# Kernel optimization log

Hardware: AMD Instinct MI355X
Metric: run time of the kernel (lower is better)

The kernel has to match this reference:

```python
import jax, jax.numpy as jnp
import numpy as np

CAP_FACTOR = 1.25


def _moe_top1(x, wg, w1, b1, w2, b2):
    """Top-1 switch MoE with capacity-based token dropping.
    x: [T, d]; wg: [d, E]; w1: [E, d, f]; b1: [E, f]; w2: [E, f, d]; b2: [E, d].
    """
    T, d = x.shape
    E = wg.shape[1]
    cap = int(CAP_FACTOR * T / E)
    probs = jax.nn.softmax(x @ wg, axis=-1)            # [T, E]
    idx = jnp.argmax(probs, axis=-1)                   # [T] expert assignment
    gate = jnp.max(probs, axis=-1)                     # [T] gate prob
    oh = jax.nn.one_hot(idx, E, dtype=jnp.int32)       # [T, E]
    # position of each token within its expert's buffer
    pos = (jnp.cumsum(oh, axis=0) * oh).sum(-1) - 1    # [T]
    keep = pos < cap                                   # drop tokens over capacity
    pos_w = jnp.where(keep, pos, cap)                  # dropped -> overflow slot
    # dispatch: scatter tokens into per-expert buffers [E, cap+1, d]
    buf = jnp.zeros((E, cap + 1, d), dtype=x.dtype).at[idx, pos_w].set(x)
    buf = buf[:, :cap]                                 # slice off overflow slot
    # grouped expert FFN
    h = jax.nn.relu(jnp.einsum('ecd,edf->ecf', buf, w1) + b1[:, None, :])
    eo = jnp.einsum('ecf,efd->ecd', h, w2) + b2[:, None, :]
    # combine: gather each token's expert output, scale by gate prob, zero dropped
    pos_g = jnp.minimum(pos_w, cap - 1)
    out = eo[idx, pos_g] * (gate * keep.astype(x.dtype))[:, None]
    return out


def setup_inputs():
    key = jax.random.key(0)
    ks = jax.random.split(key, 12)
    B, S, d, dff, E1, E2 = 8, 2048, 1024, 4096, 8, 16
    s = lambda fan: np.float32(1.0 / np.sqrt(fan))
    return dict(
        x=jax.random.normal(ks[0], (B, S, d), jnp.float32),
        y=jax.random.randint(ks[1], (B,), 0, d),
        wg1=jax.random.normal(ks[2], (d, E1), jnp.float32) * s(d),
        w1a=jax.random.normal(ks[3], (E1, d, dff), jnp.float32) * s(d),
        b1a=jnp.zeros((E1, dff), jnp.float32),
        w2a=jax.random.normal(ks[4], (E1, dff, d), jnp.float32) * s(dff),
        b2a=jnp.zeros((E1, d), jnp.float32),
        wg2=jax.random.normal(ks[5], (d, E2), jnp.float32) * s(d),
        w1b=jax.random.normal(ks[6], (E2, d, dff), jnp.float32) * s(d),
        b1b=jnp.zeros((E2, dff), jnp.float32),
        w2b=jax.random.normal(ks[7], (E2, dff, d), jnp.float32) * s(dff),
        b2b=jnp.zeros((E2, d), jnp.float32),
    )


def reference(x, y, wg1, w1a, b1a, w2a, b2a, wg2, w1b, b1b, w2b, b2b):
    B, S, d = x.shape
    xf = x.reshape(B * S, d)
    m1 = _moe_top1(xf, wg1, w1a, b1a, w2a, b2a)        # moe1(x)
    m2 = _moe_top1(m1, wg2, w1b, b1b, w2b, b2b)        # moe2(moe_out)
    resid = x + m2.reshape(B, S, d)                    # residual add
    sent = resid.mean(axis=1)                          # [B, d] mean-pool -> logits
    logp = jax.nn.log_softmax(sent, axis=-1)
    return -logp[jnp.arange(B), y].mean()              # cross-entropy loss
```

## Files before the change

### kernel.cpp

```cpp
#include <hip/hip_runtime.h>
#include <hip/hip_bf16.h>
#include <cstdint>
#include <cstddef>

#define B_    8
#define S_    2048
#define D_    1024
#define DFF_  4096
#define E1_   8
#define E2_   16
#define T_    (B_*S_)
#define CAP1_ 2560
#define CAP2_ 1280
#define EC_   20480

typedef float f32x4 __attribute__((ext_vector_type(4)));

__device__ __forceinline__ unsigned int pk4fp8(float a, float b, float c, float d) {
  int r = __builtin_amdgcn_cvt_pk_fp8_f32(a, b, 0, false);
  r = __builtin_amdgcn_cvt_pk_fp8_f32(c, d, r, true);
  return (unsigned int)r;
}

template<int E>
__global__ __launch_bounds__(256)
void gate_kernel(const float* __restrict__ X, const float* __restrict__ WG,
                 int* __restrict__ idxO, float* __restrict__ gateO) {
  const int lane = threadIdx.x & 63;
  const int wv   = threadIdx.x >> 6;
  const int t    = blockIdx.x * 4 + wv;
  const float* xr = X + (size_t)t * D_;
  float acc[E];
#pragma unroll
  for (int e = 0; e < E; ++e) acc[e] = 0.f;
#pragma unroll
  for (int i = 0; i < 4; ++i) {
    float4 xv = *(const float4*)(xr + i * 256 + lane * 4);
    int kb = i * 256 + lane * 4;
#pragma unroll
    for (int j = 0; j < 4; ++j) {
      float xs = (&xv.x)[j];
      const float* wr = WG + (size_t)(kb + j) * E;
#pragma unroll
      for (int e = 0; e < E; ++e) acc[e] += xs * wr[e];
    }
  }
#pragma unroll
  for (int e = 0; e < E; ++e) {
    float v = acc[e];
#pragma unroll
    for (int s = 32; s >= 1; s >>= 1) v += __shfl_xor(v, s, 64);
    acc[e] = v;
  }
  if (lane == 0) {
    float mx = acc[0]; int mi = 0;
#pragma unroll
    for (int e = 1; e < E; ++e) if (acc[e] > mx) { mx = acc[e]; mi = e; }
    float s = 0.f;
#pragma unroll
    for (int e = 0; e < E; ++e) s += expf(acc[e] - mx);
    idxO[t]  = mi;
    gateO[t] = 1.0f / s;
  }
}

__global__ __launch_bounds__(1024)
void scan_kernel(const int* __restrict__ idx, int E, int cap,
                 int* __restrict__ pos, int* __restrict__ kept) {
  __shared__ int cnt[16][17];
  __shared__ int gbase[16];
  const int tid = threadIdx.x;
  const int w = tid >> 6, lane = tid & 63;
  if (tid < E) gbase[tid] = 0;
  __syncthreads();
  const unsigned long long lt = (lane == 63) ? 0xFFFFFFFFFFFFFFFFull >> 1
                                             : ((1ull << lane) - 1ull);
  for (int it = 0; it < T_ / 1024; ++it) {
    int t = it * 1024 + tid;
    int mi = idx[t];
    int rank = 0;
    for (int e = 0; e < E; ++e) {
      unsigned long long m = __ballot(mi == e);
      if (lane == 0) cnt[w][e] = __popcll(m);
      if (mi == e) rank = __popcll(m & lt);
    }
    __syncthreads();
    int off = 0;
    for (int w2 = 0; w2 < w; ++w2) off += cnt[w2][mi];
    pos[t] = gbase[mi] + off + rank;
    __syncthreads();
    if (tid < E) {
      int tot = 0;
      for (int w2 = 0; w2 < 16; ++w2) tot += cnt[w2][tid];
      gbase[tid] += tot;
    }
    __syncthreads();
  }
  if (tid < E) kept[tid] = min(gbase[tid], cap);
}

__global__ __launch_bounds__(64)
void scatter_kernel(const float* __restrict__ X, const int* __restrict__ idx,
                    const int* __restrict__ pos, int cap,
                    unsigned char* __restrict__ xbuf, int* __restrict__ tokmap,
                    float* __restrict__ mzero) {
  const int t = blockIdx.x;
  const int lane = threadIdx.x;
  const int p = pos[t];
  if (p < cap) {
    const size_t dst = ((size_t)idx[t] * cap + p) * D_;
    const float* xr = X + (size_t)t * D_;
#pragma unroll
    for (int i = 0; i < 4; ++i) {
      float4 v = *(const float4*)(xr + i * 256 + lane * 4);
      *(unsigned int*)(xbuf + dst + i * 256 + lane * 4) = pk4fp8(v.x, v.y, v.z, v.w);
    }
    if (lane == 0) tokmap[(size_t)idx[t] * cap + p] = t;
  } else {
    float4 z = {0.f, 0.f, 0.f, 0.f};
    float* mr = mzero + (size_t)t * D_;
#pragma unroll
    for (int i = 0; i < 4; ++i) *(float4*)(mr + i * 256 + lane * 4) = z;
  }
}

__global__ __launch_bounds__(256)
void wtrans_kernel(const float* __restrict__ src, unsigned char* __restrict__ dst,
                   int K, int N) {
  __shared__ float t[64][65];
  const int tid = threadIdx.x;
  const size_t eo = (size_t)blockIdx.z * K * N;
  const int k0 = blockIdx.y * 64, n0 = blockIdx.x * 64;
  const float* s = src + eo + (size_t)k0 * N + n0;
  unsigned char* d = dst + eo + (size_t)n0 * K + k0;
#pragma unroll
  for (int i = 0; i < 4; ++i) {
    int k = i * 16 + (tid >> 4);
    int n4 = (tid & 15) * 4;
    float4 v = *(const float4*)(s + (size_t)k * N + n4);
    t[k][n4] = v.x; t[k][n4 + 1] = v.y; t[k][n4 + 2] = v.z; t[k][n4 + 3] = v.w;
  }
  __syncthreads();
#pragma unroll
  for (int i = 0; i < 4; ++i) {
    int n = i * 16 + (tid >> 4);
    int k4 = (tid & 15) * 4;
    *(unsigned int*)(d + (size_t)n * K + k4) =
        pk4fp8(t[k4][n], t[k4 + 1][n], t[k4 + 2][n], t[k4 + 3][n]);
  }
}

#define STG(BASEPTR, H, KT, SLOT) do {                                          \
    const unsigned char* _s = (BASEPTR) + (size_t)((H) * 128) * K + (KT) + st_off; \
    __builtin_amdgcn_global_load_lds((const __attribute__((address_space(1))) void*)_s, \
        (__attribute__((address_space(3))) void*)(smem + (SLOT) + dst0), 16, 0, 0);   \
    __builtin_amdgcn_global_load_lds((const __attribute__((address_space(1))) void*)(_s + (size_t)64 * K), \
        (__attribute__((address_space(3))) void*)(smem + (SLOT) + 8192 + dst0), 16, 0, 0); \
  } while (0)

#define RDA(BUF, MH) do { _Pragma("unroll")                                     \
    for (int m_ = 0; m_ < 4; ++m_) {                                            \
      const char* _p = smem + (BUF) * 65536 + aslot + ((MH) * 4 + m_) * 2048 + vaf; \
      _Pragma("unroll") for (int k_ = 0; k_ < 4; ++k_)                          \
        af[m_][k_] = *(const long long*)(_p + (((2 * k_ + c0) ^ swz7) << 4)); } } while (0)

#define RDB01(BUF, DEST) do { _Pragma("unroll")                                 \
    for (int j_ = 0; j_ < 2; ++j_) {                                            \
      const char* _p = smem + (BUF) * 65536 + bslot + j_ * 2048 + vbf;          \
      _Pragma("unroll") for (int k_ = 0; k_ < 4; ++k_)                          \
        DEST[j_][k_] = *(const long long*)(_p + (((2 * k_ + c0) ^ swz7) << 4)); } } while (0)

#define RDB23(BUF) do { _Pragma("unroll")                                       \
    for (int j_ = 0; j_ < 2; ++j_) {                                            \
      const char* _p = smem + (BUF) * 65536 + bslot + (2 + j_) * 2048 + vbf;    \
      _Pragma("unroll") for (int k_ = 0; k_ < 4; ++k_)                          \
        bfb[j_][k_] = *(const long long*)(_p + (((2 * k_ + c0) ^ swz7) << 4)); } } while (0)

#define QUADN0(MH, BA) do {                                                     \
    __builtin_amdgcn_s_setprio(1);                                              \
    _Pragma("unroll") for (int m_ = 0; m_ < 4; ++m_)                            \
    _Pragma("unroll") for (int j_ = 0; j_ < 2; ++j_)                            \
    _Pragma("unroll") for (int k_ = 0; k_ < 4; ++k_)                            \
      acc[(MH) * 4 + m_][j_] = __builtin_amdgcn_mfma_f32_16x16x32_fp8_fp8(      \
          af[m_][k_], BA[j_][k_], acc[(MH) * 4 + m_][j_], 0, 0, 0);             \
    __builtin_amdgcn_s_setprio(0);                                              \
  } while (0)

#define QUADN1(MH) do {                                                         \
    __builtin_amdgcn_s_setprio(1);                                              \
    _Pragma("unroll") for (int m_ = 0; m_ < 4; ++m_)                            \
    _Pragma("unroll") for (int j_ = 0; j_ < 2; ++j_)                            \
    _Pragma("unroll") for (int k_ = 0; k_ < 4; ++k_)                            \
      acc[(MH) * 4 + m_][2 + j_] = __builtin_amdgcn_mfma_f32_16x16x32_fp8_fp8(  \
          af[m_][k_], bfb[j_][k_], acc[(MH) * 4 + m_][2 + j_], 0, 0, 0);        \
    __builtin_amdgcn_s_setprio(0);                                              \
  } while (0)

#define SB0   __builtin_amdgcn_sched_barrier(0)
#define BAR   __builtin_amdgcn_s_barrier()
#define VM6   do { asm volatile("s_waitcnt vmcnt(6)" ::: "memory"); SB0; } while (0)
#define VM8   do { asm volatile("s_waitcnt vmcnt(8)" ::: "memory"); SB0; } while (0)
#define VM0   do { asm volatile("s_waitcnt vmcnt(0)" ::: "memory"); SB0; } while (0)

template<int MODE>
__global__ __launch_bounds__(512, 2)
void moe_gemm(const unsigned char* __restrict__ A,
              const unsigned char* __restrict__ BT,
              const float* __restrict__ bias, int K, int N, int cap, int nbcnt,
              int ntl,
              const int* __restrict__ kept,
              unsigned char* __restrict__ Hout, float* __restrict__ Mout,
              const int* __restrict__ tokmap, const float* __restrict__ gate,
              const float* __restrict__ tsrc, unsigned char* __restrict__ tdst,
              int tK, int tN, int tE, int nwrk) {
  __shared__ char smem[131072];
  const int tid  = threadIdx.x;

  if (tsrc != nullptr && (int)blockIdx.x < nwrk) {
    const int ntn = tN >> 7, ntk = tK >> 7;
    const int tiles = tE * ntk * ntn;
    const int krow = tid >> 2;
    const int kq   = (tid & 3) * 32;
    for (int t = blockIdx.x; t < tiles; t += nwrk) {
      const int e2 = t / (ntk * ntn), rm = t - e2 * (ntk * ntn);
      const int k0 = (rm / ntn) << 7, n0 = (rm - (rm / ntn) * ntn) << 7;
      const float* s = tsrc + (size_t)e2 * tK * tN + (size_t)(k0 + krow) * tN + n0 + kq;
#pragma unroll
      for (int j = 0; j < 8; ++j) {
        float4 v = *(const float4*)(s + j * 4);
        unsigned int q = pk4fp8(v.x, v.y, v.z, v.w);
#pragma unroll
        for (int b = 0; b < 4; ++b)
          smem[(kq + j * 4 + b) * 128 + krow] = (char)((q >> (8 * b)) & 0xff);
      }
      __syncthreads();
      unsigned char* d = tdst + (size_t)e2 * tK * tN + (size_t)(n0 + krow) * tK + k0 + kq;
      *(uint4*)(d)      = *(const uint4*)(smem + krow * 128 + kq);
      *(uint4*)(d + 16) = *(const uint4*)(smem + krow * 128 + kq + 16);
      __syncthreads();
    }
    return;
  }

  const int gbid = (int)blockIdx.x - (tsrc ? nwrk : 0);
  const int lane = tid & 63;
  const int wv   = tid >> 6;
  const int wr   = wv >> 2;
  const int wc   = wv & 3;

  const int wg  = (gbid & 7) * (ntl >> 3) + (gbid >> 3);
  const int per_grp = nbcnt * 4;
  const int grp = wg / per_grp;
  const int rem = wg - grp * per_grp;
  const int mb  = grp * 4 + (rem & 3);
  const int nb  = rem >> 2;

  const int e  = (mb * 256) / cap;
  const int r0 = mb * 256 - e * cap;
  const int kept_e = kept[e];
  if (r0 >= kept_e) return;
  const unsigned char* Ab = A + (size_t)(mb * 256) * K;
  const unsigned char* Bb = BT + ((size_t)e * N + (size_t)nb * 256) * K;

  f32x4 acc[8][4];
#pragma unroll
  for (int m = 0; m < 8; ++m)
#pragma unroll
    for (int n = 0; n < 4; ++n) acc[m][n] = (f32x4){0.f, 0.f, 0.f, 0.f};

  const int scol   = ((tid & 7) ^ ((tid >> 3) & 7)) * 16;
  const size_t st_off = (size_t)(tid >> 3) * K + scol;
  const int dst0   = tid * 16;

  const int r16  = lane & 15;
  const int l34  = lane >> 4;
  const int c0   = l34 >> 1;
  const int swz7 = r16 & 7;
  const int vaf  = r16 * 128 + (l34 & 1) * 8;
  const int vbf  = (wc & 1) * 8192 + vaf;
  const int aslot = wr * 16384;
  const int bslot = 32768 + (wc >> 1) * 16384;
  long long af[4][4], bA0[2][4], bA1[2][4], bfb[2][4];

  STG(Ab, 0, 0, 0);
  STG(Bb, 0, 0, 32768);
  STG(Bb, 1, 0, 49152);
  STG(Ab, 1, 0, 16384);
  STG(Ab, 0, 128, 65536);
  STG(Bb, 0, 128, 98304);
  STG(Bb, 1, 128, 114688);
  STG(Ab, 1, 128, 81920);
  VM8; BAR;
  RDB01(0, bA0);

  const int NT = K >> 7;
  const int NI = K >> 8;
  for (int i = 0; i < NI; ++i) {
    const bool last = (i == NI - 1);
    const bool s2 = (2 * i + 2) < NT;
    const bool s3 = (2 * i + 3) < NT;
    const int kt1 = (2 * i + 1) << 7;
    const int kt2 = (2 * i + 2) << 7;
    const int kt3 = (2 * i + 3) << 7;

    RDA(0, 0);
    if (i > 0) STG(Ab, 1, kt1, 81920);
    BAR; QUADN0(0, bA0); BAR;
    RDB23(0);
    if (s2) STG(Ab, 0, kt2, 0);
    BAR; QUADN1(0); BAR;
    RDA(0, 1);
    if (s2) STG(Bb, 0, kt2, 32768);
    BAR; QUADN1(1); BAR;
    if (s2) STG(Bb, 1, kt2, 49152);
    if (last) { VM0; } else { VM6; }
    RDB01(1, bA1);
    BAR; QUADN0(1, bA0); BAR;
    RDA(1, 0);
    if (s2) STG(Ab, 1, kt2, 16384);
    BAR; QUADN0(0, bA1); BAR;
    RDB23(1);
    if (s3) STG(Ab, 0, kt3, 65536);
    BAR; QUADN1(0); BAR;
    RDA(1, 1);
    if (s3) STG(Bb, 0, kt3, 98304);
    BAR; QUADN1(1); BAR;
    if (s3) STG(Bb, 1, kt3, 114688);
    if (!last) { VM6; RDB01(0, bA0); }
    BAR; QUADN0(1, bA1); BAR;
  }

  const int rg = lane >> 4;
  float bv[4];
#pragma unroll
  for (int n = 0; n < 4; ++n)
    bv[n] = bias[(size_t)e * N + nb * 256 + wc * 64 + n * 16 + r16];

#pragma unroll
  for (int m = 0; m < 8; ++m) {
#pragma unroll
    for (int r = 0; r < 4; ++r) {
      const int lrow = wr * 128 + m * 16 + rg * 4 + r;
      if (MODE == 0) {
        unsigned char* orow = Hout + (size_t)(mb * 256 + lrow) * N + nb * 256;
        unsigned int q = pk4fp8(fmaxf(acc[m][0][r] + bv[0], 0.f),
                                fmaxf(acc[m][1][r] + bv[1], 0.f),
                                fmaxf(acc[m][2][r] + bv[2], 0.f),
                                fmaxf(acc[m][3][r] + bv[3], 0.f));
        orow[wc * 64 +  0 + r16] = (unsigned char)(q & 0xff);
        orow[wc * 64 + 16 + r16] = (unsigned char)((q >> 8) & 0xff);
        orow[wc * 64 + 32 + r16] = (unsigned char)((q >> 16) & 0xff);
        orow[wc * 64 + 48 + r16] = (unsigned char)(q >> 24);
      } else {
        const int lr = r0 + lrow;
        if (lr < kept_e) {
          const int tok = tokmap[mb * 256 + lrow];
          const float gsc = gate[tok];
          float* orow = Mout + (size_t)tok * N + nb * 256;
#pragma unroll
          for (int n = 0; n < 4; ++n)
            orow[wc * 64 + n * 16 + r16] = (acc[m][n][r] + bv[n]) * gsc;
        }
      }
    }
  }
}

__global__ __launch_bounds__(256)
void reduce_kernel(const float* __restrict__ X, const float* __restrict__ M2,
                   float* __restrict__ sent) {
  const int c = blockIdx.x * 256 + threadIdx.x;
  const int b = blockIdx.z;
  const int s0 = blockIdx.y * 128;
  float a = 0.f;
  size_t base = ((size_t)b * S_ + s0) * D_ + c;
  for (int s = 0; s < 128; ++s) a += X[base + (size_t)s * D_] + M2[base + (size_t)s * D_];
  atomicAdd(&sent[b * D_ + c], a * (1.0f / (float)S_));
}

__global__ __launch_bounds__(64)
void loss_kernel(const float* __restrict__ sent, const int* __restrict__ y,
                 float* __restrict__ out) {
  const int lane = threadIdx.x;
  float total = 0.f;
  for (int b = 0; b < B_; ++b) {
    const float* s = sent + b * D_;
    float v[16];
    float mx = -1e30f;
#pragma unroll
    for (int i = 0; i < 16; ++i) { v[i] = s[lane + i * 64]; mx = fmaxf(mx, v[i]); }
#pragma unroll
    for (int sh = 32; sh >= 1; sh >>= 1) mx = fmaxf(mx, __shfl_xor(mx, sh, 64));
    float sm = 0.f;
#pragma unroll
    for (int i = 0; i < 16; ++i) sm += expf(v[i] - mx);
#pragma unroll
    for (int sh = 32; sh >= 1; sh >>= 1) sm += __shfl_xor(sm, sh, 64);
    total += logf(sm) + mx - s[y[b]];
  }
  if (lane == 0) out[0] = total * (1.0f / (float)B_);
}

extern "C" void kernel_launch(void* const* d_in, const int* in_sizes, int n_in,
                              void* d_out, int out_size, void* d_ws, size_t ws_size,
                              hipStream_t stream) {
  const float* x   = (const float*)d_in[0];
  const int*   y   = (const int*)d_in[1];
  const float* wg1 = (const float*)d_in[2];
  const float* w1a = (const float*)d_in[3];
  const float* b1a = (const float*)d_in[4];
  const float* w2a = (const float*)d_in[5];
  const float* b2a = (const float*)d_in[6];
  const float* wg2 = (const float*)d_in[7];
  const float* w1b = (const float*)d_in[8];
  const float* b1b = (const float*)d_in[9];
  const float* w2b = (const float*)d_in[10];
  const float* b2b = (const float*)d_in[11];
  float* out = (float*)d_out;
  (void)in_sizes; (void)n_in; (void)out_size; (void)ws_size;

  char* base = (char*)d_ws;
  size_t o = 0;
  auto alloc = [&](size_t bytes) { size_t r = o; o = (o + bytes + 255) & ~(size_t)255; return r; };
  int*   idx1    = (int*)  (base + alloc((size_t)T_ * 4));
  int*   pos1    = (int*)  (base + alloc((size_t)T_ * 4));
  float* gate1   = (float*)(base + alloc((size_t)T_ * 4));
  int*   idx2    = (int*)  (base + alloc((size_t)T_ * 4));
  int*   pos2    = (int*)  (base + alloc((size_t)T_ * 4));
  float* gate2   = (float*)(base + alloc((size_t)T_ * 4));
  int*   kept1   = (int*)  (base + alloc(64 * 4));
  int*   kept2   = (int*)  (base + alloc(64 * 4));
  int*   tokmap1 = (int*)  (base + alloc((size_t)EC_ * 4));
  int*   tokmap2 = (int*)  (base + alloc((size_t)EC_ * 4));
  float* sent    = (float*)(base + alloc((size_t)B_ * D_ * 4));
  float* m1      = (float*)(base + alloc((size_t)T_ * D_ * 4));
  unsigned char* xbuf = (unsigned char*)(base + alloc((size_t)EC_ * D_));
  unsigned char* h    = (unsigned char*)(base + alloc((size_t)EC_ * DFF_));
  unsigned char* P1   = (unsigned char*)(base + alloc((size_t)E2_ * D_ * DFF_));
  unsigned char* P2   = (unsigned char*)(base + alloc((size_t)E2_ * D_ * DFF_));

  hipMemsetAsync(sent, 0, (size_t)B_ * D_ * 4, stream);

  const int NT0 = (DFF_ / 256) * (EC_ / 256);
  const int NT1 = (D_  / 256) * (EC_ / 256);
  const int NW  = 128;

  gate_kernel<E1_><<<T_ / 4, 256, 0, stream>>>(x, wg1, idx1, gate1);
  scan_kernel<<<1, 1024, 0, stream>>>(idx1, E1_, CAP1_, pos1, kept1);
  scatter_kernel<<<T_, 64, 0, stream>>>(x, idx1, pos1, CAP1_, xbuf, tokmap1, m1);
  wtrans_kernel<<<dim3(DFF_ / 64, D_ / 64, E1_), 256, 0, stream>>>(w1a, P1, D_, DFF_);
  moe_gemm<0><<<NT0 + NW, 512, 0, stream>>>(
      xbuf, P1, b1a, D_, DFF_, CAP1_, DFF_ / 256, NT0, kept1, h, nullptr, nullptr, nullptr,
      w2a, P2, DFF_, D_, E1_, NW);
  moe_gemm<1><<<NT1 + NW, 512, 0, stream>>>(
      h, P2, b2a, DFF_, D_, CAP1_, D_ / 256, NT1, kept1, nullptr, m1, tokmap1, gate1,
      w1b, P1, D_, DFF_, E2_, NW);

  gate_kernel<E2_><<<T_ / 4, 256, 0, stream>>>(m1, wg2, idx2, gate2);
  scan_kernel<<<1, 1024, 0, stream>>>(idx2, E2_, CAP2_, pos2, kept2);
  scatter_kernel<<<T_, 64, 0, stream>>>(m1, idx2, pos2, CAP2_, xbuf, tokmap2, m1);
  moe_gemm<0><<<NT0 + NW, 512, 0, stream>>>(
      xbuf, P1, b1b, D_, DFF_, CAP2_, DFF_ / 256, NT0, kept2, h, nullptr, nullptr, nullptr,
      w2b, P2, DFF_, D_, E2_, NW);
  moe_gemm<1><<<NT1, 512, 0, stream>>>(
      h, P2, b2b, DFF_, D_, CAP2_, D_ / 256, NT1, kept2, nullptr, m1, tokmap2, gate2,
      nullptr, nullptr, 0, 0, 0, 0);

  reduce_kernel<<<dim3(D_ / 256, S_ / 128, B_), 256, 0, stream>>>(x, m1, sent);
  loss_kernel<<<1, 64, 0, stream>>>(sent, y, out);
}
```

Baseline: 1.246 ms.

## Fuse weight transpose into gate kernel and overlap x-sum with final GEMM

Removes the standalone wtrans kernel: the fp8 transpose of w1a now runs in extra worker blocks appended to the first gate kernel, so it overlaps gating. The residual mean of x is moved into 64 extra blocks of the last expert GEMM, so reduce_kernel only reads m2. Scatter now packs four tokens per 256-thread block to cut the block count. The aim is to hide the transpose and half the reduce traffic behind other work, at the cost of extra blocks competing with the main kernels.

```diff
diff --git a/kernel.cpp b/kernel.cpp
--- a/kernel.cpp
+++ b/kernel.cpp
@@ -25,10 +25,43 @@
 template<int E>
 __global__ __launch_bounds__(256)
 void gate_kernel(const float* __restrict__ X, const float* __restrict__ WG,
-                 int* __restrict__ idxO, float* __restrict__ gateO) {
-  const int lane = threadIdx.x & 63;
-  const int wv   = threadIdx.x >> 6;
-  const int t    = blockIdx.x * 4 + wv;
+                 int* __restrict__ idxO, float* __restrict__ gateO,
+                 const float* __restrict__ tsrc, unsigned char* __restrict__ tdst,
+                 int tK, int tN, int tE, int nwrk) {
+  __shared__ char tsm[16384];
+  const int tid = threadIdx.x;
+
+  if (tsrc != nullptr && (int)blockIdx.x < nwrk) {
+    const int ntn = tN >> 7, ntk = tK >> 7;
+    const int tiles = tE * ntk * ntn;
+    const int krow = tid >> 1;
+    const int kq   = (tid & 1) * 64;
+    for (int t = blockIdx.x; t < tiles; t += nwrk) {
+      const int e2 = t / (ntk * ntn), rm = t - e2 * (ntk * ntn);
+      const int k0 = (rm / ntn) << 7, n0 = (rm - (rm / ntn) * ntn) << 7;
+      const float* s = tsrc + (size_t)e2 * tK * tN + (size_t)(k0 + krow) * tN + n0 + kq;
+#pragma unroll
+      for (int j = 0; j < 16; ++j) {
+        float4 v = *(const float4*)(s + j * 4);
+        unsigned int q = pk4fp8(v.x, v.y, v.z, v.w);
+#pragma unroll
+        for (int b = 0; b < 4; ++b)
+          tsm[(kq + j * 4 + b) * 128 + krow] = (char)((q >> (8 * b)) & 0xff);
+      }
+      __syncthreads();
+      unsigned char* d = tdst + (size_t)e2 * tK * tN + (size_t)(n0 + krow) * tK + k0 + kq;
+#pragma unroll
+      for (int i = 0; i < 4; ++i)
+        *(uint4*)(d + 16 * i) = *(const uint4*)(tsm + krow * 128 + kq + 16 * i);
+      __syncthreads();
+    }
+    return;
+  }
+
+  const int gb   = (int)blockIdx.x - ((tsrc != nullptr) ? nwrk : 0);
+  const int lane = tid & 63;
+  const int wv   = tid >> 6;
+  const int t    = gb * 4 + wv;
   const float* xr = X + (size_t)t * D_;
   float acc[E];
 #pragma unroll
@@ -99,13 +132,13 @@
   if (tid < E) kept[tid] = min(gbase[tid], cap);
 }
 
-__global__ __launch_bounds__(64)
+__global__ __launch_bounds__(256)
 void scatter_kernel(const float* __restrict__ X, const int* __restrict__ idx,
                     const int* __restrict__ pos, int cap,
                     unsigned char* __restrict__ xbuf, int* __restrict__ tokmap,
                     float* __restrict__ mzero) {
-  const int t = blockIdx.x;
-  const int lane = threadIdx.x;
+  const int t = blockIdx.x * 4 + (threadIdx.x >> 6);
+  const int lane = threadIdx.x & 63;
   const int p = pos[t];
   if (p < cap) {
     const size_t dst = ((size_t)idx[t] * cap + p) * D_;
@@ -121,32 +154,6 @@
     float* mr = mzero + (size_t)t * D_;
 #pragma unroll
     for (int i = 0; i < 4; ++i) *(float4*)(mr + i * 256 + lane * 4) = z;
-  }
-}
-
-__global__ __launch_bounds__(256)
-void wtrans_kernel(const float* __restrict__ src, unsigned char* __restrict__ dst,
-                   int K, int N) {
-  __shared__ float t[64][65];
-  const int tid = threadIdx.x;
-  const size_t eo = (size_t)blockIdx.z * K * N;
-  const int k0 = blockIdx.y * 64, n0 = blockIdx.x * 64;
-  const float* s = src + eo + (size_t)k0 * N + n0;
-  unsigned char* d = dst + eo + (size_t)n0 * K + k0;
-#pragma unroll
-  for (int i = 0; i < 4; ++i) {
-    int k = i * 16 + (tid >> 4);
-    int n4 = (tid & 15) * 4;
-    float4 v = *(const float4*)(s + (size_t)k * N + n4);
-    t[k][n4] = v.x; t[k][n4 + 1] = v.y; t[k][n4 + 2] = v.z; t[k][n4 + 3] = v.w;
-  }
-  __syncthreads();
-#pragma unroll
-  for (int i = 0; i < 4; ++i) {
-    int n = i * 16 + (tid >> 4);
-    int k4 = (tid & 15) * 4;
-    *(unsigned int*)(d + (size_t)n * K + k4) =
-        pk4fp8(t[k4][n], t[k4 + 1][n], t[k4 + 2][n], t[k4 + 3][n]);
   }
 }
 
@@ -212,7 +219,9 @@
               unsigned char* __restrict__ Hout, float* __restrict__ Mout,
               const int* __restrict__ tokmap, const float* __restrict__ gate,
               const float* __restrict__ tsrc, unsigned char* __restrict__ tdst,
-              int tK, int tN, int tE, int nwrk) {
+              int tK, int tN, int tE,
+              const float* __restrict__ xsrc, float* __restrict__ sentx,
+              int nwrk) {
   __shared__ char smem[131072];
   const int tid  = threadIdx.x;
 
@@ -242,7 +251,22 @@
     return;
   }
 
-  const int gbid = (int)blockIdx.x - (tsrc ? nwrk : 0);
+  if (xsrc != nullptr && (int)blockIdx.x < nwrk) {
+    const int b  = blockIdx.x >> 3;
+    const int se = blockIdx.x & 7;
+    const float* xr = xsrc + ((size_t)b * S_ + (size_t)se * 256) * D_;
+    float ax = 0.f, ay = 0.f;
+    const int c2 = tid * 2;
+    for (int s = 0; s < 256; ++s) {
+      float2 v = *(const float2*)(xr + (size_t)s * D_ + c2);
+      ax += v.x; ay += v.y;
+    }
+    atomicAdd(&sentx[b * D_ + c2],     ax * (1.0f / (float)S_));
+    atomicAdd(&sentx[b * D_ + c2 + 1], ay * (1.0f / (float)S_));
+    return;
+  }
+
+  const int gbid = (int)blockIdx.x - ((tsrc != nullptr || xsrc != nullptr) ? nwrk : 0);
   const int lane = tid & 63;
   const int wv   = tid >> 6;
   const int wr   = wv >> 2;
@@ -367,14 +391,13 @@
 }
 
 __global__ __launch_bounds__(256)
-void reduce_kernel(const float* __restrict__ X, const float* __restrict__ M2,
-                   float* __restrict__ sent) {
+void reduce_kernel(const float* __restrict__ M2, float* __restrict__ sent) {
   const int c = blockIdx.x * 256 + threadIdx.x;
   const int b = blockIdx.z;
   const int s0 = blockIdx.y * 128;
   float a = 0.f;
   size_t base = ((size_t)b * S_ + s0) * D_ + c;
-  for (int s = 0; s < 128; ++s) a += X[base + (size_t)s * D_] + M2[base + (size_t)s * D_];
+  for (int s = 0; s < 128; ++s) a += M2[base + (size_t)s * D_];
   atomicAdd(&sent[b * D_ + c], a * (1.0f / (float)S_));
 }
 
@@ -445,27 +468,28 @@
   const int NT1 = (D_  / 256) * (EC_ / 256);
   const int NW  = 128;
 
-  gate_kernel<E1_><<<T_ / 4, 256, 0, stream>>>(x, wg1, idx1, gate1);
+  gate_kernel<E1_><<<T_ / 4 + NW, 256, 0, stream>>>(x, wg1, idx1, gate1,
+                                                    w1a, P1, D_, DFF_, E1_, NW);
   scan_kernel<<<1, 1024, 0, stream>>>(idx1, E1_, CAP1_, pos1, kept1);
-  scatter_kernel<<<T_, 64, 0, stream>>>(x, idx1, pos1, CAP1_, xbuf, tokmap1, m1);
-  wtrans_kernel<<<dim3(DFF_ / 64, D_ / 64, E1_), 256, 0, stream>>>(w1a, P1, D_, DFF_);
+  scatter_kernel<<<T_ / 4, 256, 0, stream>>>(x, idx1, pos1, CAP1_, xbuf, tokmap1, m1);
   moe_gemm<0><<<NT0 + NW, 512, 0, stream>>>(
       xbuf, P1, b1a, D_, DFF_, CAP1_, DFF_ / 256, NT0, kept1, h, nullptr, nullptr, nullptr,
-      w2a, P2, DFF_, D_, E1_, NW);
+      w2a, P2, DFF_, D_, E1_, nullptr, nullptr, NW);
   moe_gemm<1><<<NT1 + NW, 512, 0, stream>>>(
       h, P2, b2a, DFF_, D_, CAP1_, D_ / 256, NT1, kept1, nullptr, m1, tokmap1, gate1,
-      w1b, P1, D_, DFF_, E2_, NW);
-
-  gate_kernel<E2_><<<T_ / 4, 256, 0, stream>>>(m1, wg2, idx2, gate2);
+      w1b, P1, D_, DFF_, E2_, nullptr, nullptr, NW);
+
+  gate_kernel<E2_><<<T_ / 4, 256, 0, stream>>>(m1, wg2, idx2, gate2,
+                                               nullptr, nullptr, 0, 0, 0, 0);
   scan_kernel<<<1, 1024, 0, stream>>>(idx2, E2_, CAP2_, pos2, kept2);
-  scatter_kernel<<<T_, 64, 0, stream>>>(m1, idx2, pos2, CAP2_, xbuf, tokmap2, m1);
+  scatter_kernel<<<T_ / 4, 256, 0, stream>>>(m1, idx2, pos2, CAP2_, xbuf, tokmap2, m1);
   moe_gemm<0><<<NT0 + NW, 512, 0, stream>>>(
       xbuf, P1, b1b, D_, DFF_, CAP2_, DFF_ / 256, NT0, kept2, h, nullptr, nullptr, nullptr,
-      w2b, P2, DFF_, D_, E2_, NW);
-  moe_gemm<1><<<NT1, 512, 0, stream>>>(
+      w2b, P2, DFF_, D_, E2_, nullptr, nullptr, NW);
+  moe_gemm<1><<<NT1 + 64, 512, 0, stream>>>(
       h, P2, b2b, DFF_, D_, CAP2_, D_ / 256, NT1, kept2, nullptr, m1, tokmap2, gate2,
-      nullptr, nullptr, 0, 0, 0, 0);
-
-  reduce_kernel<<<dim3(D_ / 256, S_ / 128, B_), 256, 0, stream>>>(x, m1, sent);
+      nullptr, nullptr, 0, 0, 0, x, sent, 64);
+
+  reduce_kernel<<<dim3(D_ / 256, S_ / 128, B_), 256, 0, stream>>>(m1, sent);
   loss_kernel<<<1, 64, 0, stream>>>(sent, y, out);
 }
```

New measurement: 1.257 ms. Within noise of the previous version (+0.9%).
